# Optimization experiments

Measured on AMD Instinct MI355X. Metric: run time of the kernel, lower is better.

The kernel has to match this reference:

```python
import jax, jax.numpy as jnp
import numpy as np

N_NODES = 100000
N_EDGES = 800000
IN_DIM = 128
HIDDEN_DIM = 256
OUT_DIM = 40


def setup_inputs() -> dict:
    key = jax.random.key(0)
    k_x, k_e, k_w1, k_w2 = jax.random.split(key, 4)
    x = jax.random.normal(k_x, (N_NODES, IN_DIM), dtype=jnp.float32)
    edge_index = jax.random.randint(k_e, (2, N_EDGES), 0, N_NODES, dtype=jnp.int32)
    # Glorot-style init like PyG GCNConv
    s1 = 1.0 / np.sqrt(IN_DIM)
    s2 = 1.0 / np.sqrt(HIDDEN_DIM)
    W1 = jax.random.uniform(k_w1, (IN_DIM, HIDDEN_DIM), dtype=jnp.float32, minval=-s1, maxval=s1)
    b1 = jnp.zeros((HIDDEN_DIM,), dtype=jnp.float32)
    W2 = jax.random.uniform(k_w2, (HIDDEN_DIM, OUT_DIM), dtype=jnp.float32, minval=-s2, maxval=s2)
    b2 = jnp.zeros((OUT_DIM,), dtype=jnp.float32)
    return {"x": x, "edge_index": edge_index, "W1": W1, "b1": b1, "W2": W2, "b2": b2}


def _gcn_conv(x, W, b, src, dst, n_nodes):
    # PyG GCNConv: linear transform, add self-loops, symmetric normalization,
    # scatter-add aggregation, then bias.
    h = x @ W  # [N, F_out]
    loops = jnp.arange(n_nodes, dtype=src.dtype)
    s = jnp.concatenate([src, loops])  # [E+N]
    d = jnp.concatenate([dst, loops])
    deg = jax.ops.segment_sum(jnp.ones_like(d, dtype=h.dtype), d, num_segments=n_nodes)
    dinv = jax.lax.rsqrt(jnp.maximum(deg, 1.0))  # deg >= 1 with self-loops
    norm = dinv[s] * dinv[d]  # [E+N]
    msgs = h[s] * norm[:, None]  # [E+N, F_out] -- dominant memory traffic
    out = jax.ops.segment_sum(msgs, d, num_segments=n_nodes)
    return out + b


def reference(x, edge_index, W1, b1, W2, b2):
    src, dst = edge_index[0], edge_index[1]
    n = x.shape[0]
    h = _gcn_conv(x, W1, b1, src, dst, n)
    h = jax.nn.relu(h)
    # dropout is identity in eval mode
    h = _gcn_conv(h, W2, b2, src, dst, n)
    return jax.nn.log_softmax(h, axis=1)
```

## Files before the change

### kernel.cpp

```cpp
#include <hip/hip_runtime.h>
#include <math.h>

#define N_NODES 100000
#define N_EDGES 800000
#define IN_DIM 128
#define HIDDEN_DIM 256
#define OUT_DIM 40
#define CAP 32
#define SHARD_DIV 12500
#define NPAIRS (N_NODES * 64)
#define T1 (HIDDEN_DIM * IN_DIM)
#define T2 (64 * HIDDEN_DIM)

typedef __attribute__((ext_vector_type(8))) __bf16 bf16x8;
typedef __attribute__((ext_vector_type(4))) float f32x4;

#define FIXSC 131072.0f
#define FIXSC_INV 7.62939453125e-6f

__device__ __forceinline__ unsigned short f2bf(float f) {
    unsigned u = __float_as_uint(f);
    unsigned r = (u + 0x7FFFu + ((u >> 16) & 1u)) >> 16;
    return (unsigned short)r;
}
__device__ __forceinline__ float bflo(unsigned v) { return __uint_as_float(v << 16); }
__device__ __forceinline__ float bfhi(unsigned v) { return __uint_as_float(v & 0xFFFF0000u); }

__device__ __forceinline__ bf16x8 ld_frag16(const unsigned short* p) {
    union { uint4 u; bf16x8 b; } t;
    t.u = *(const uint4*)p;
    return t.b;
}

__global__ __launch_bounds__(256) void fill_kernel(const int* __restrict__ src,
                                                   const int* __restrict__ dst,
                                                   int* __restrict__ cnt,
                                                   int* __restrict__ esrc, int e) {
    int shard = blockIdx.x & 7;
    int i = (blockIdx.x >> 3) * 256 + threadIdx.x;
    if (i < e) {
        int d = dst[i];
        if (d / SHARD_DIV == shard) {
            int p = atomicAdd(&cnt[d], 1);
            if (p < CAP) esrc[d * CAP + p] = src[i];
        }
    }
}

__global__ __launch_bounds__(256) void cast_kernel(const float* __restrict__ x,
                                                   const int* __restrict__ cnt,
                                                   unsigned* __restrict__ xs,
                                                   const float* __restrict__ W1,
                                                   unsigned short* __restrict__ W1t,
                                                   const float* __restrict__ W2,
                                                   unsigned short* __restrict__ W2t) {
    int i = blockIdx.x * 256 + threadIdx.x;
    if (i < NPAIRS) {
        float dn = rsqrtf((float)cnt[i >> 6] + 1.0f) * FIXSC;
        float2 v = ((const float2*)x)[i];
        xs[i] = (unsigned)f2bf(v.x * dn) | ((unsigned)f2bf(v.y * dn) << 16);
    }
    if (i < T1) {
        int n = i >> 7, k = i & 127;
        W1t[i] = f2bf(W1[(size_t)k * HIDDEN_DIM + n]);
    } else if (i < T1 + T2) {
        int j = i - T1;
        int n = j >> 8, k = j & 255;
        float v = (n < OUT_DIM) ? W2[(size_t)k * OUT_DIM + n] : 0.0f;
        W2t[j] = f2bf(v);
    }
}

__global__ __launch_bounds__(256) void aggx_kernel(const unsigned* __restrict__ xs,
                                                   const int* __restrict__ cnt,
                                                   const int* __restrict__ esrc,
                                                   unsigned* __restrict__ aggxb, int n) {
    int wid = (blockIdx.x * 256 + threadIdx.x) >> 6;
    int lane = threadIdx.x & 63;
    if (wid >= n) return;
    int c = cnt[wid];
    int m = c < CAP ? c : CAP;
    unsigned v = xs[(size_t)wid * 64 + lane];
    int ia = (int)bflo(v), ib = (int)bfhi(v);
    int base = wid * CAP;
    int j = 0;
    for (; j + 7 < m; j += 8) {
        int s0 = esrc[base + j],     s1 = esrc[base + j + 1];
        int s2 = esrc[base + j + 2], s3 = esrc[base + j + 3];
        int s4 = esrc[base + j + 4], s5 = esrc[base + j + 5];
        int s6 = esrc[base + j + 6], s7 = esrc[base + j + 7];
        unsigned u0 = xs[(size_t)s0 * 64 + lane];
        unsigned u1 = xs[(size_t)s1 * 64 + lane];
        unsigned u2 = xs[(size_t)s2 * 64 + lane];
        unsigned u3 = xs[(size_t)s3 * 64 + lane];
        unsigned u4 = xs[(size_t)s4 * 64 + lane];
        unsigned u5 = xs[(size_t)s5 * 64 + lane];
        unsigned u6 = xs[(size_t)s6 * 64 + lane];
        unsigned u7 = xs[(size_t)s7 * 64 + lane];
        ia += ((int)bflo(u0) + (int)bflo(u1)) + ((int)bflo(u2) + (int)bflo(u3))
            + ((int)bflo(u4) + (int)bflo(u5)) + ((int)bflo(u6) + (int)bflo(u7));
        ib += ((int)bfhi(u0) + (int)bfhi(u1)) + ((int)bfhi(u2) + (int)bfhi(u3))
            + ((int)bfhi(u4) + (int)bfhi(u5)) + ((int)bfhi(u6) + (int)bfhi(u7));
    }
    for (; j + 3 < m; j += 4) {
        int s0 = esrc[base + j],     s1 = esrc[base + j + 1];
        int s2 = esrc[base + j + 2], s3 = esrc[base + j + 3];
        unsigned u0 = xs[(size_t)s0 * 64 + lane];
        unsigned u1 = xs[(size_t)s1 * 64 + lane];
        unsigned u2 = xs[(size_t)s2 * 64 + lane];
        unsigned u3 = xs[(size_t)s3 * 64 + lane];
        ia += ((int)bflo(u0) + (int)bflo(u1)) + ((int)bflo(u2) + (int)bflo(u3));
        ib += ((int)bfhi(u0) + (int)bfhi(u1)) + ((int)bfhi(u2) + (int)bfhi(u3));
    }
    for (; j < m; j++) {
        unsigned u = xs[(size_t)esrc[base + j] * 64 + lane];
        ia += (int)bflo(u); ib += (int)bfhi(u);
    }
    float k = rsqrtf((float)c + 1.0f) * FIXSC_INV;
    float ax = (float)ia * k, ay = (float)ib * k;
    aggxb[(size_t)wid * 64 + lane] = (unsigned)f2bf(ax) | ((unsigned)f2bf(ay) << 16);
}

#define BSTR 136
#define HSTR 72
__global__ __launch_bounds__(256) void gemm12_kernel(const unsigned short* __restrict__ A,
                                                     const unsigned short* __restrict__ W1t,
                                                     const unsigned short* __restrict__ W2t,
                                                     const float* __restrict__ b1,
                                                     const int* __restrict__ cnt,
                                                     unsigned short* __restrict__ h2s,
                                                     int M) {
    __shared__ __align__(16) unsigned short Bs[256 * BSTR];
    __shared__ __align__(16) unsigned short Hs[4 * 16 * HSTR];
    int tid = threadIdx.x;
    int wv = tid >> 6, lane = tid & 63;
    int quad = lane >> 4, l16 = lane & 15;
    int row0 = blockIdx.x * 64 + wv * 16;

#pragma unroll
    for (int rep = 0; rep < 16; rep++) {
        int lin = rep * 256 + tid;
        int row = lin >> 4, ch = lin & 15;
        *(uint4*)&Bs[row * BSTR + ch * 8] = *(const uint4*)&W1t[(size_t)row * 128 + ch * 8];
    }

    float bv[16];
#pragma unroll
    for (int ct = 0; ct < 16; ct++) bv[ct] = b1[ct * 16 + l16];

    f32x4 zero4 = {0.f, 0.f, 0.f, 0.f};
    f32x4 acc[16];
#pragma unroll
    for (int ct = 0; ct < 16; ct++) acc[ct] = zero4;

    __syncthreads();

#pragma unroll
    for (int k0 = 0; k0 < 128; k0 += 32) {
        int gm = row0 + l16;
        union { uint4 u; bf16x8 b; } cv;
        cv.u = make_uint4(0u, 0u, 0u, 0u);
        if (gm < M) cv.u = *(const uint4*)&A[(size_t)gm * 128 + k0 + quad * 8];
        bf16x8 af = cv.b;
#pragma unroll
        for (int ct = 0; ct < 16; ct++) {
            bf16x8 bfr = ld_frag16(&Bs[(ct * 16 + l16) * BSTR + k0 + quad * 8]);
            acc[ct] = __builtin_amdgcn_mfma_f32_16x16x32_bf16(af, bfr, acc[ct], 0, 0, 0);
        }
    }

    unsigned short* hw = &Hs[wv * 16 * HSTR];
    f32x4 acc2[4];
#pragma unroll
    for (int c2 = 0; c2 < 4; c2++) acc2[c2] = zero4;

#pragma unroll
    for (int chunk = 0; chunk < 4; chunk++) {
#pragma unroll
        for (int cc = 0; cc < 4; cc++) {
            int ct = chunk * 4 + cc;
#pragma unroll
            for (int r = 0; r < 4; r++) {
                int row = quad * 4 + r;
                float v = fmaxf(acc[ct][r] + bv[ct], 0.0f);
                hw[row * HSTR + cc * 16 + l16] = f2bf(v);
            }
        }
#pragma unroll
        for (int kk = 0; kk < 2; kk++) {
            bf16x8 af2 = ld_frag16(&hw[l16 * HSTR + kk * 32 + quad * 8]);
#pragma unroll
            for (int c2 = 0; c2 < 4; c2++) {
                bf16x8 bfr = ld_frag16(&W2t[(size_t)(c2 * 16 + l16) * 256 + chunk * 64 + kk * 32 + quad * 8]);
                acc2[c2] = __builtin_amdgcn_mfma_f32_16x16x32_bf16(af2, bfr, acc2[c2], 0, 0, 0);
            }
        }
    }

#pragma unroll
    for (int c2 = 0; c2 < 4; c2++) {
        int col = c2 * 16 + l16;
#pragma unroll
        for (int r = 0; r < 4; r++) {
            int gm = row0 + quad * 4 + r;
            if (gm < M) {
                float v = acc2[c2][r] * (rsqrtf((float)cnt[gm] + 1.0f) * FIXSC);
                h2s[(size_t)gm * 64 + col] = f2bf(v);
            }
        }
    }
}

__global__ __launch_bounds__(256) void agg2_kernel(const unsigned* __restrict__ h2u,
                                                   const int* __restrict__ cnt,
                                                   const int* __restrict__ esrc,
                                                   const float* __restrict__ b2,
                                                   float* __restrict__ out, int n) {
    int wave = (blockIdx.x * 256 + threadIdx.x) >> 6;
    int lane = threadIdx.x & 63;
    int half = lane >> 5, l32 = lane & 31;
    int node = wave * 2 + half;
    if (node >= n) return;
    int c = cnt[node];
    int m = c < CAP ? c : CAP;
    int base = node * CAP;
    unsigned v = h2u[(size_t)node * 32 + l32];
    int ia = (int)bflo(v), ib = (int)bfhi(v);
    int j = 0;
    for (; j + 7 < m; j += 8) {
        int s0 = esrc[base + j],     s1 = esrc[base + j + 1];
        int s2 = esrc[base + j + 2], s3 = esrc[base + j + 3];
        int s4 = esrc[base + j + 4], s5 = esrc[base + j + 5];
        int s6 = esrc[base + j + 6], s7 = esrc[base + j + 7];
        unsigned u0 = h2u[(size_t)s0 * 32 + l32];
        unsigned u1 = h2u[(size_t)s1 * 32 + l32];
        unsigned u2 = h2u[(size_t)s2 * 32 + l32];
        unsigned u3 = h2u[(size_t)s3 * 32 + l32];
        unsigned u4 = h2u[(size_t)s4 * 32 + l32];
        unsigned u5 = h2u[(size_t)s5 * 32 + l32];
        unsigned u6 = h2u[(size_t)s6 * 32 + l32];
        unsigned u7 = h2u[(size_t)s7 * 32 + l32];
        ia += ((int)bflo(u0) + (int)bflo(u1)) + ((int)bflo(u2) + (int)bflo(u3))
            + ((int)bflo(u4) + (int)bflo(u5)) + ((int)bflo(u6) + (int)bflo(u7));
        ib += ((int)bfhi(u0) + (int)bfhi(u1)) + ((int)bfhi(u2) + (int)bfhi(u3))
            + ((int)bfhi(u4) + (int)bfhi(u5)) + ((int)bfhi(u6) + (int)bfhi(u7));
    }
    for (; j + 3 < m; j += 4) {
        int s0 = esrc[base + j],     s1 = esrc[base + j + 1];
        int s2 = esrc[base + j + 2], s3 = esrc[base + j + 3];
        unsigned u0 = h2u[(size_t)s0 * 32 + l32];
        unsigned u1 = h2u[(size_t)s1 * 32 + l32];
        unsigned u2 = h2u[(size_t)s2 * 32 + l32];
        unsigned u3 = h2u[(size_t)s3 * 32 + l32];
        ia += ((int)bflo(u0) + (int)bflo(u1)) + ((int)bflo(u2) + (int)bflo(u3));
        ib += ((int)bfhi(u0) + (int)bfhi(u1)) + ((int)bfhi(u2) + (int)bfhi(u3));
    }
    for (; j < m; j++) {
        unsigned u = h2u[(size_t)esrc[base + j] * 32 + l32];
        ia += (int)bflo(u); ib += (int)bfhi(u);
    }
    float k = rsqrtf((float)c + 1.0f) * FIXSC_INV;
    int f0 = 2 * l32;
    bool a0 = (f0 < OUT_DIM), a1 = (f0 + 1 < OUT_DIM);
    float v0 = a0 ? fmaf((float)ia, k, b2[f0]) : -INFINITY;
    float v1 = a1 ? fmaf((float)ib, k, b2[f0 + 1]) : -INFINITY;
    float mx = fmaxf(v0, v1);
#pragma unroll
    for (int o = 16; o > 0; o >>= 1) mx = fmaxf(mx, __shfl_xor(mx, o));
    float e = (a0 ? __expf(v0 - mx) : 0.0f) + (a1 ? __expf(v1 - mx) : 0.0f);
#pragma unroll
    for (int o = 16; o > 0; o >>= 1) e += __shfl_xor(e, o);
    if (a0) {
        float ls = __logf(e);
        *(float2*)&out[(size_t)node * OUT_DIM + f0] = make_float2(v0 - mx - ls, v1 - mx - ls);
    }
}

extern "C" void kernel_launch(void* const* d_in, const int* in_sizes, int n_in,
                              void* d_out, int out_size, void* d_ws, size_t ws_size,
                              hipStream_t stream) {
    const float* x  = (const float*)d_in[0];
    const int* ei   = (const int*)d_in[1];
    const float* W1 = (const float*)d_in[2];
    const float* b1 = (const float*)d_in[3];
    const float* W2 = (const float*)d_in[4];
    const float* b2 = (const float*)d_in[5];
    float* out = (float*)d_out;

    const int* src = ei;
    const int* dst = ei + N_EDGES;

    char* ws = (char*)d_ws;
    size_t off = 0;
    auto carve = [&](size_t bytes) -> char* {
        char* p = ws + off;
        off = (off + bytes + 255) & ~(size_t)255;
        return p;
    };
    int*      cnt   = (int*)     carve((size_t)N_NODES * 4);
    int*      esrc  = (int*)     carve((size_t)N_NODES * CAP * 4);
    unsigned* xs    = (unsigned*)carve((size_t)N_NODES * 64 * 4);
    unsigned short* W1t = (unsigned short*)carve((size_t)T1 * 2);
    unsigned short* W2t = (unsigned short*)carve((size_t)T2 * 2);
    unsigned* aggxb = (unsigned*)carve((size_t)N_NODES * 64 * 4);
    unsigned short* h2s = (unsigned short*)carve((size_t)N_NODES * 64 * 2);

    hipMemsetAsync(cnt, 0, (size_t)N_NODES * 4, stream);
    fill_kernel<<<((N_EDGES + 255) / 256) * 8, 256, 0, stream>>>(src, dst, cnt, esrc, N_EDGES);
    cast_kernel<<<(NPAIRS + 255) / 256, 256, 0, stream>>>(x, cnt, xs, W1, W1t, W2, W2t);
    aggx_kernel<<<(N_NODES * 64 + 255) / 256, 256, 0, stream>>>(xs, cnt, esrc, aggxb, N_NODES);
    gemm12_kernel<<<(N_NODES + 63) / 64, 256, 0, stream>>>(
        (const unsigned short*)aggxb, W1t, W2t, b1, cnt, h2s, N_NODES);
    agg2_kernel<<<((N_NODES + 1) / 2 * 64 + 255) / 256, 256, 0, stream>>>(
        (const unsigned*)h2s, cnt, esrc, b2, out, N_NODES);
}
```

Baseline: 265.2 us.

## Compute two row tiles per wave and pre-swizzle W2 into MFMA fragment layout

Each wave in the fused GEMM kernel now computes 32 rows as two 16-row tiles. Every W1 fragment read from LDS therefore feeds two MFMAs, halving the LDS reads per output, and the grid is halved to match. The cast kernel writes W2 in per-lane MFMA fragment order so the second GEMM loads it with contiguous 16-byte reads. The second GEMM also computes only 3 column tiles (48 columns) instead of 4, since the output has 40. The cost is higher accumulator register pressure (launch bounds set to 2 blocks) and fewer blocks in flight.

```diff
diff --git a/kernel.cpp b/kernel.cpp
--- a/kernel.cpp
+++ b/kernel.cpp
@@ -53,7 +53,7 @@
                                                    const float* __restrict__ W1,
                                                    unsigned short* __restrict__ W1t,
                                                    const float* __restrict__ W2,
-                                                   unsigned short* __restrict__ W2t) {
+                                                   unsigned short* __restrict__ W2f) {
     int i = blockIdx.x * 256 + threadIdx.x;
     if (i < NPAIRS) {
         float dn = rsqrtf((float)cnt[i >> 6] + 1.0f) * FIXSC;
@@ -65,9 +65,13 @@
         W1t[i] = f2bf(W1[(size_t)k * HIDDEN_DIM + n]);
     } else if (i < T1 + T2) {
         int j = i - T1;
-        int n = j >> 8, k = j & 255;
+        int e = j & 7, lane = (j >> 3) & 63, frag = j >> 9;
+        int l16 = lane & 15, quad = lane >> 4;
+        int c2 = frag >> 3, chunk = (frag >> 1) & 3, kk = frag & 1;
+        int n = c2 * 16 + l16;
+        int k = chunk * 64 + kk * 32 + quad * 8 + e;
         float v = (n < OUT_DIM) ? W2[(size_t)k * OUT_DIM + n] : 0.0f;
-        W2t[j] = f2bf(v);
+        W2f[j] = f2bf(v);
     }
 }
 
@@ -123,19 +127,66 @@
 
 #define BSTR 136
 #define HSTR 72
-__global__ __launch_bounds__(256) void gemm12_kernel(const unsigned short* __restrict__ A,
-                                                     const unsigned short* __restrict__ W1t,
-                                                     const unsigned short* __restrict__ W2t,
-                                                     const float* __restrict__ b1,
-                                                     const int* __restrict__ cnt,
-                                                     unsigned short* __restrict__ h2s,
-                                                     int M) {
+__device__ __forceinline__ void phase2_epi(f32x4 (&acc)[16], int rowg,
+                                           unsigned short* hw,
+                                           const unsigned short* __restrict__ W2f,
+                                           const float* __restrict__ b1,
+                                           const int* __restrict__ cnt,
+                                           unsigned short* __restrict__ h2s,
+                                           int lane, int quad, int l16, int M) {
+    f32x4 acc2[3];
+#pragma unroll
+    for (int c2 = 0; c2 < 3; c2++) acc2[c2] = (f32x4){0.f, 0.f, 0.f, 0.f};
+#pragma unroll
+    for (int chunk = 0; chunk < 4; chunk++) {
+#pragma unroll
+        for (int cc = 0; cc < 4; cc++) {
+            int ct = chunk * 4 + cc;
+            float bb = b1[ct * 16 + l16];
+#pragma unroll
+            for (int r = 0; r < 4; r++) {
+                int row = quad * 4 + r;
+                float v = fmaxf(acc[ct][r] + bb, 0.0f);
+                hw[row * HSTR + cc * 16 + l16] = f2bf(v);
+            }
+        }
+#pragma unroll
+        for (int kk = 0; kk < 2; kk++) {
+            bf16x8 af2 = ld_frag16(&hw[l16 * HSTR + kk * 32 + quad * 8]);
+#pragma unroll
+            for (int c2 = 0; c2 < 3; c2++) {
+                bf16x8 bfr = ld_frag16(&W2f[(size_t)((c2 * 8 + chunk * 2 + kk) * 64 + lane) * 8]);
+                acc2[c2] = __builtin_amdgcn_mfma_f32_16x16x32_bf16(af2, bfr, acc2[c2], 0, 0, 0);
+            }
+        }
+    }
+#pragma unroll
+    for (int c2 = 0; c2 < 3; c2++) {
+        int col = c2 * 16 + l16;
+#pragma unroll
+        for (int r = 0; r < 4; r++) {
+            int gm = rowg + quad * 4 + r;
+            if (gm < M) {
+                float v = acc2[c2][r] * (rsqrtf((float)cnt[gm] + 1.0f) * FIXSC);
+                h2s[(size_t)gm * 64 + col] = f2bf(v);
+            }
+        }
+    }
+}
+
+__global__ __launch_bounds__(256, 2) void gemm12_kernel(const unsigned short* __restrict__ A,
+                                                        const unsigned short* __restrict__ W1t,
+                                                        const unsigned short* __restrict__ W2f,
+                                                        const float* __restrict__ b1,
+                                                        const int* __restrict__ cnt,
+                                                        unsigned short* __restrict__ h2s,
+                                                        int M) {
     __shared__ __align__(16) unsigned short Bs[256 * BSTR];
     __shared__ __align__(16) unsigned short Hs[4 * 16 * HSTR];
     int tid = threadIdx.x;
     int wv = tid >> 6, lane = tid & 63;
     int quad = lane >> 4, l16 = lane & 15;
-    int row0 = blockIdx.x * 64 + wv * 16;
+    int row0 = blockIdx.x * 128 + wv * 32;
 
 #pragma unroll
     for (int rep = 0; rep < 16; rep++) {
@@ -144,71 +195,32 @@
         *(uint4*)&Bs[row * BSTR + ch * 8] = *(const uint4*)&W1t[(size_t)row * 128 + ch * 8];
     }
 
-    float bv[16];
-#pragma unroll
-    for (int ct = 0; ct < 16; ct++) bv[ct] = b1[ct * 16 + l16];
-
     f32x4 zero4 = {0.f, 0.f, 0.f, 0.f};
-    f32x4 acc[16];
-#pragma unroll
-    for (int ct = 0; ct < 16; ct++) acc[ct] = zero4;
+    f32x4 accA[16], accB[16];
+#pragma unroll
+    for (int ct = 0; ct < 16; ct++) { accA[ct] = zero4; accB[ct] = zero4; }
 
     __syncthreads();
 
 #pragma unroll
     for (int k0 = 0; k0 < 128; k0 += 32) {
-        int gm = row0 + l16;
-        union { uint4 u; bf16x8 b; } cv;
-        cv.u = make_uint4(0u, 0u, 0u, 0u);
-        if (gm < M) cv.u = *(const uint4*)&A[(size_t)gm * 128 + k0 + quad * 8];
-        bf16x8 af = cv.b;
+        int gmA = row0 + l16, gmB = row0 + 16 + l16;
+        union { uint4 u; bf16x8 b; } cvA, cvB;
+        cvA.u = make_uint4(0u, 0u, 0u, 0u);
+        cvB.u = make_uint4(0u, 0u, 0u, 0u);
+        if (gmA < M) cvA.u = *(const uint4*)&A[(size_t)gmA * 128 + k0 + quad * 8];
+        if (gmB < M) cvB.u = *(const uint4*)&A[(size_t)gmB * 128 + k0 + quad * 8];
 #pragma unroll
         for (int ct = 0; ct < 16; ct++) {
             bf16x8 bfr = ld_frag16(&Bs[(ct * 16 + l16) * BSTR + k0 + quad * 8]);
-            acc[ct] = __builtin_amdgcn_mfma_f32_16x16x32_bf16(af, bfr, acc[ct], 0, 0, 0);
+            accA[ct] = __builtin_amdgcn_mfma_f32_16x16x32_bf16(cvA.b, bfr, accA[ct], 0, 0, 0);
+            accB[ct] = __builtin_amdgcn_mfma_f32_16x16x32_bf16(cvB.b, bfr, accB[ct], 0, 0, 0);
         }
     }
 
     unsigned short* hw = &Hs[wv * 16 * HSTR];
-    f32x4 acc2[4];
-#pragma unroll
-    for (int c2 = 0; c2 < 4; c2++) acc2[c2] = zero4;
-
-#pragma unroll
-    for (int chunk = 0; chunk < 4; chunk++) {
-#pragma unroll
-        for (int cc = 0; cc < 4; cc++) {
-            int ct = chunk * 4 + cc;
-#pragma unroll
-            for (int r = 0; r < 4; r++) {
-                int row = quad * 4 + r;
-                float v = fmaxf(acc[ct][r] + bv[ct], 0.0f);
-                hw[row * HSTR + cc * 16 + l16] = f2bf(v);
-            }
-        }
-#pragma unroll
-        for (int kk = 0; kk < 2; kk++) {
-            bf16x8 af2 = ld_frag16(&hw[l16 * HSTR + kk * 32 + quad * 8]);
-#pragma unroll
-            for (int c2 = 0; c2 < 4; c2++) {
-                bf16x8 bfr = ld_frag16(&W2t[(size_t)(c2 * 16 + l16) * 256 + chunk * 64 + kk * 32 + quad * 8]);
-                acc2[c2] = __builtin_amdgcn_mfma_f32_16x16x32_bf16(af2, bfr, acc2[c2], 0, 0, 0);
-            }
-        }
-    }
-
-#pragma unroll
-    for (int c2 = 0; c2 < 4; c2++) {
-        int col = c2 * 16 + l16;
-#pragma unroll
-        for (int r = 0; r < 4; r++) {
-            int gm = row0 + quad * 4 + r;
-            if (gm < M) {
-                float v = acc2[c2][r] * (rsqrtf((float)cnt[gm] + 1.0f) * FIXSC);
-                h2s[(size_t)gm * 64 + col] = f2bf(v);
-            }
-        }
-    }
+    phase2_epi(accA, row0,      hw, W2f, b1, cnt, h2s, lane, quad, l16, M);
+    phase2_epi(accB, row0 + 16, hw, W2f, b1, cnt, h2s, lane, quad, l16, M);
 }
 
 __global__ __launch_bounds__(256) void agg2_kernel(const unsigned* __restrict__ h2u,
@@ -301,16 +313,16 @@
     int*      esrc  = (int*)     carve((size_t)N_NODES * CAP * 4);
     unsigned* xs    = (unsigned*)carve((size_t)N_NODES * 64 * 4);
     unsigned short* W1t = (unsigned short*)carve((size_t)T1 * 2);
-    unsigned short* W2t = (unsigned short*)carve((size_t)T2 * 2);
+    unsigned short* W2f = (unsigned short*)carve((size_t)T2 * 2);
     unsigned* aggxb = (unsigned*)carve((size_t)N_NODES * 64 * 4);
     unsigned short* h2s = (unsigned short*)carve((size_t)N_NODES * 64 * 2);
 
     hipMemsetAsync(cnt, 0, (size_t)N_NODES * 4, stream);
     fill_kernel<<<((N_EDGES + 255) / 256) * 8, 256, 0, stream>>>(src, dst, cnt, esrc, N_EDGES);
-    cast_kernel<<<(NPAIRS + 255) / 256, 256, 0, stream>>>(x, cnt, xs, W1, W1t, W2, W2t);
+    cast_kernel<<<(NPAIRS + 255) / 256, 256, 0, stream>>>(x, cnt, xs, W1, W1t, W2, W2f);
     aggx_kernel<<<(N_NODES * 64 + 255) / 256, 256, 0, stream>>>(xs, cnt, esrc, aggxb, N_NODES);
-    gemm12_kernel<<<(N_NODES + 63) / 64, 256, 0, stream>>>(
-        (const unsigned short*)aggxb, W1t, W2t, b1, cnt, h2s, N_NODES);
+    gemm12_kernel<<<(N_NODES + 127) / 128, 256, 0, stream>>>(
+        (const unsigned short*)aggxb, W1t, W2f, b1, cnt, h2s, N_NODES);
     agg2_kernel<<<((N_NODES + 1) / 2 * 64 + 255) / 256, 256, 0, stream>>>(
         (const unsigned*)h2s, cnt, esrc, b2, out, N_NODES);
 }
```

New measurement: 245.7 us. 1.08x faster.
